# Kernel tuning notes

Measured on AMD Instinct MI355X. Metric: run time of the kernel, lower is better.

The kernel has to match this reference:

```python
import jax, jax.numpy as jnp
import numpy as np

B, F, H, W = 1, 4, 20, 44
P = H * W            # 880 tokens per frame (20*44, from max_attention_size = 15*880)
S = F * P            # 3520 packed tokens
DIM, NH, FFN, OUT = 1536, 12, 6144, 64   # OUT = prod(patch_size)*out_dim = 4*16
HD = DIM // NH       # 128
C = HD // 2          # 64 rotary complex pairs
EPS = 1e-6


def _rope_angles():
    # Wan 3D RoPE: split C pairs as (C-2*(C//3), C//3, C//3) over (frame, h, w)
    cf, ch, cw = C - 2 * (C // 3), C // 3, C // 3
    def tab(n, cp):
        inv = 1.0 / (10000.0 ** (np.arange(cp) / cp))
        return np.outer(np.arange(n), inv)
    af = np.broadcast_to(tab(F, cf)[:, None, None, :], (F, H, W, cf))
    ah = np.broadcast_to(tab(H, ch)[None, :, None, :], (F, H, W, ch))
    aw = np.broadcast_to(tab(W, cw)[None, None, :, :], (F, H, W, cw))
    return np.concatenate([af, ah, aw], -1).reshape(S, C).astype(np.float32)


def setup_inputs() -> dict:
    key = jax.random.key(0)
    ks = jax.random.split(key, 24)
    g = lambda i, shape, s=0.02: jax.random.normal(ks[i], shape, dtype=jnp.float32) * s
    inp = {
        'x': jax.random.normal(ks[0], (B, S, DIM), dtype=jnp.float32),
        'e': g(1, (B, F, 6, DIM), 1.0),
        'e_head': g(2, (B, F, 2, DIM), 1.0),
        'rope_angles': jnp.asarray(_rope_angles()),
        'mod_block': g(3, (1, 6, DIM), 1.0 / float(np.sqrt(DIM))),
        'mod_head': g(4, (1, 2, DIM), 1.0 / float(np.sqrt(DIM))),
        'Wq': g(5, (DIM, DIM)), 'bq': jnp.zeros((DIM,), jnp.float32),
        'Wk': g(6, (DIM, DIM)), 'bk': jnp.zeros((DIM,), jnp.float32),
        'Wv': g(7, (DIM, DIM)), 'bv': jnp.zeros((DIM,), jnp.float32),
        'Wo': g(8, (DIM, DIM)), 'bo': jnp.zeros((DIM,), jnp.float32),
        'wq_norm': jnp.ones((DIM,), jnp.float32),
        'wk_norm': jnp.ones((DIM,), jnp.float32),
        'W1': g(9, (DIM, FFN)), 'b1': jnp.zeros((FFN,), jnp.float32),
        'W2': g(10, (FFN, DIM)), 'b2': jnp.zeros((DIM,), jnp.float32),
        'Wh': g(11, (DIM, OUT)), 'bh': jnp.zeros((OUT,), jnp.float32),
    }
    return inp


def _ln(x):
    # WanLayerNorm without elementwise affine
    m = jnp.mean(x, axis=-1, keepdims=True)
    v = jnp.var(x, axis=-1, keepdims=True)
    return (x - m) * jax.lax.rsqrt(v + EPS)


def _rms(x, w):
    return x * jax.lax.rsqrt(jnp.mean(x * x, axis=-1, keepdims=True) + EPS) * w


def _rope(t, ang):
    # t: [B,S,NH,HD]; adjacent pairs form complex numbers (view_as_complex style)
    tr = t.reshape(B, S, NH, C, 2)
    cos = jnp.cos(ang)[None, :, None, :]
    sin = jnp.sin(ang)[None, :, None, :]
    t0, t1 = tr[..., 0], tr[..., 1]
    return jnp.stack([t0 * cos - t1 * sin, t0 * sin + t1 * cos], -1).reshape(B, S, NH, HD)


def reference(x, e, e_head, rope_angles, mod_block, mod_head,
              Wq, bq, Wk, bk, Wv, bv, Wo, bo, wq_norm, wk_norm,
              W1, b1, W2, b2, Wh, bh):
    # ---- AdaLN modulation split (6-way) ----
    em = mod_block[:, None] + e                      # [B,F,6,DIM]
    e0, e1, e2, e3, e4, e5 = [em[:, :, i][:, :, None, :] for i in range(6)]

    xf = x.reshape(B, F, P, DIM)
    h = (_ln(xf) * (1 + e1) + e0).reshape(B, S, DIM)

    # ---- QK-RMSNorm + RoPE self attention (block-causal, block = one frame) ----
    q = _rope(_rms(h @ Wq + bq, wq_norm).reshape(B, S, NH, HD), rope_angles)
    k = _rope(_rms(h @ Wk + bk, wk_norm).reshape(B, S, NH, HD), rope_angles)
    v = (h @ Wv + bv).reshape(B, S, NH, HD)

    blk = jnp.arange(S) // P
    mask = blk[None, :] <= blk[:, None]              # [S,S] block-causal
    scores = jnp.einsum('bqhd,bkhd->bhqk', q, k) / np.float32(np.sqrt(HD))
    scores = jnp.where(mask[None, None], scores, jnp.float32(-1e30))
    attn = jax.nn.softmax(scores, axis=-1)
    y = jnp.einsum('bhqk,bkhd->bqhd', attn, v).reshape(B, S, DIM) @ Wo + bo

    xf = xf + y.reshape(B, F, P, DIM) * e2

    # ---- FFN with AdaLN modulation ----
    hf = (_ln(xf) * (1 + e4) + e3).reshape(B, S, DIM)
    ff = jax.nn.gelu(hf @ W1 + b1) @ W2 + b2
    xf = xf + ff.reshape(B, F, P, DIM) * e5

    # ---- OutputHead: modulated norm + linear ----
    eh = mod_head[:, None] + e_head                  # [B,F,2,DIM]
    eh0 = eh[:, :, 0][:, :, None, :]
    eh1 = eh[:, :, 1][:, :, None, :]
    out = (_ln(xf) * (1 + eh1) + eh0) @ Wh + bh      # [B,F,P,OUT]
    return out
```

## Files before the change

### kernel.cpp

```cpp
#include <hip/hip_runtime.h>
#include <cstdint>
#include <cstddef>

typedef __bf16 bf16;
typedef __bf16 bf16x2 __attribute__((ext_vector_type(2)));
typedef __bf16 bf16x8 __attribute__((ext_vector_type(8)));
typedef float f32x4 __attribute__((ext_vector_type(4)));
typedef unsigned int u32x4 __attribute__((ext_vector_type(4)));

#define S_TOK 3520
#define S_PAD 3584
#define P_TOK 880
#define NFRM 4
#define DIM 1536
#define NH 12
#define HD 128
#define FFN_D 6144
#define NOUT 64
#define EPSV 1e-6f
#define QSCALE 0.12751743f

__device__ __forceinline__ f32x4 mfma16(bf16x8 a, bf16x8 b, f32x4 c) {
  return __builtin_amdgcn_mfma_f32_16x16x32_bf16(a, b, c, 0, 0, 0);
}

__device__ __forceinline__ void gload_lds16(const bf16* g, bf16* l) {
  __builtin_amdgcn_global_load_lds(
      (const __attribute__((address_space(1))) unsigned int*)g,
      (__attribute__((address_space(3))) unsigned int*)l, 16, 0, 0);
}

__device__ __forceinline__ uint32_t pk2(float lo, float hi) {
  bf16x2 t;
  t[0] = (bf16)lo;
  t[1] = (bf16)hi;
  return __builtin_bit_cast(uint32_t, t);
}

__global__ __launch_bounds__(256) void k_prep(const float* __restrict__ e,
                                              const float* __restrict__ e_head,
                                              const float* __restrict__ mod_block,
                                              const float* __restrict__ mod_head,
                                              float* __restrict__ em,
                                              float* __restrict__ ehm) {
  int i = blockIdx.x * 256 + threadIdx.x;
  if (i < NFRM * 6 * DIM) em[i] = mod_block[i % (6 * DIM)] + e[i];
  int j = i - NFRM * 6 * DIM;
  if (j >= 0 && j < NFRM * 2 * DIM) ehm[j] = mod_head[j % (2 * DIM)] + e_head[j];
}

__global__ __launch_bounds__(256) void k_zero_vpad(bf16* __restrict__ vc) {
  size_t base = ((size_t)blockIdx.x * 28 + 27) * 4096 + 2048 + (size_t)threadIdx.x * 8;
#pragma unroll
  for (int i = 0; i < 8; ++i) vc[base + i] = (bf16)0.f;
}

__global__ __launch_bounds__(256) void k_transpose(const float* __restrict__ W,
                                                   bf16* __restrict__ Wt, int K, int N) {
  __shared__ float tile[32][33];
  int n0 = blockIdx.x * 32, k0 = blockIdx.y * 32;
  int tx = threadIdx.x & 31, ty = threadIdx.x >> 5;
#pragma unroll
  for (int j = 0; j < 4; ++j) {
    int k = k0 + ty * 4 + j;
    float v = (n0 + tx < N) ? W[(size_t)k * N + n0 + tx] : 0.f;
    tile[ty * 4 + j][tx] = v;
  }
  __syncthreads();
#pragma unroll
  for (int j = 0; j < 4; ++j) {
    int n = n0 + ty * 4 + j;
    if (n < N) Wt[(size_t)n * K + k0 + tx] = (bf16)tile[tx][ty * 4 + j];
  }
}

__global__ __launch_bounds__(256) void k_adaln(const float* __restrict__ in,
                                               bf16* __restrict__ out,
                                               const float* __restrict__ e_shift,
                                               const float* __restrict__ e_scale,
                                               int fstride) {
  int tok = blockIdx.x;
  int t = threadIdx.x;
  bf16* orow = out + (size_t)tok * DIM;
  if (tok >= S_TOK) {
#pragma unroll
    for (int i = 0; i < 6; ++i) orow[t * 6 + i] = (bf16)0.f;
    return;
  }
  const float* xrow = in + (size_t)tok * DIM;
  float v[6];
  float s = 0.f, sq = 0.f;
#pragma unroll
  for (int i = 0; i < 6; ++i) {
    v[i] = xrow[t * 6 + i];
    s += v[i];
    sq += v[i] * v[i];
  }
  for (int off = 32; off; off >>= 1) {
    s += __shfl_down(s, off);
    sq += __shfl_down(sq, off);
  }
  __shared__ float red[8];
  int wv = t >> 6, lane = t & 63;
  if (lane == 0) { red[wv] = s; red[4 + wv] = sq; }
  __syncthreads();
  float ts = red[0] + red[1] + red[2] + red[3];
  float tq = red[4] + red[5] + red[6] + red[7];
  float mean = ts * (1.f / DIM);
  float var = tq * (1.f / DIM) - mean * mean;
  float rstd = rsqrtf(var + EPSV);
  int f = tok / P_TOK;
  const float* sh = e_shift + (size_t)f * fstride;
  const float* sc = e_scale + (size_t)f * fstride;
#pragma unroll
  for (int i = 0; i < 6; ++i) {
    int d = t * 6 + i;
    orow[d] = (bf16)((v[i] - mean) * rstd * (1.f + sc[d]) + sh[d]);
  }
}

__global__ __launch_bounds__(256) void k_qkv_post(const float* __restrict__ qkv,
                                                  const float* __restrict__ wqn,
                                                  const float* __restrict__ wkn,
                                                  const float* __restrict__ ang,
                                                  bf16* __restrict__ qb,
                                                  bf16* __restrict__ kb,
                                                  bf16* __restrict__ vc) {
  int s = blockIdx.x;
  int t = threadIdx.x;
  const float* row = qkv + (size_t)s * 3 * DIM;
  float qv[6], kv[6], vv[6];
  float sqq = 0.f, sqk = 0.f;
  int d0 = t * 6;
#pragma unroll
  for (int i = 0; i < 6; ++i) {
    int d = d0 + i;
    qv[i] = row[d];
    kv[i] = row[DIM + d];
    vv[i] = row[2 * DIM + d];
    sqq += qv[i] * qv[i];
    sqk += kv[i] * kv[i];
  }
  float a1 = sqq, a2 = sqk;
  for (int off = 32; off; off >>= 1) {
    a1 += __shfl_down(a1, off);
    a2 += __shfl_down(a2, off);
  }
  __shared__ float red[8];
  int wv = t >> 6, lane = t & 63;
  if (lane == 0) { red[wv] = a1; red[4 + wv] = a2; }
  __syncthreads();
  float tq = red[0] + red[1] + red[2] + red[3];
  float tk = red[4] + red[5] + red[6] + red[7];
  float rq = rsqrtf(tq * (1.f / DIM) + EPSV);
  float rk = rsqrtf(tk * (1.f / DIM) + EPSV);
#pragma unroll
  for (int p = 0; p < 3; ++p) {
    int d = d0 + p * 2;
    int h = d >> 7;
    int hd = d & 127;
    int c = hd >> 1;
    float a = ang[(size_t)s * 64 + c];
    float sa, ca;
    sincosf(a, &sa, &ca);
    float q0 = qv[p * 2] * rq * wqn[d], q1 = qv[p * 2 + 1] * rq * wqn[d + 1];
    float k0 = kv[p * 2] * rk * wkn[d], k1 = kv[p * 2 + 1] * rk * wkn[d + 1];
    size_t base = ((size_t)h * S_TOK + s) * HD + hd;
    qb[base]     = (bf16)((q0 * ca - q1 * sa) * QSCALE);
    qb[base + 1] = (bf16)((q0 * sa + q1 * ca) * QSCALE);
    kb[base]     = (bf16)(k0 * ca - k1 * sa);
    kb[base + 1] = (bf16)(k0 * sa + k1 * ca);
  }
  int f = s / P_TOK;
  int l = s - f * P_TOK;
  int lb = l >> 5, gg = (l >> 3) & 3, r = l & 7;
#pragma unroll
  for (int i = 0; i < 6; ++i) {
    int d = d0 + i;
    int h = d >> 7, hd = d & 127;
    vc[((((size_t)(h * NFRM + f)) * 28 + lb) * 512 + gg * 128 + hd) * 8 + r] = (bf16)vv[i];
  }
}

__global__ __launch_bounds__(320) void k_attn(const bf16* __restrict__ qb,
                                              const bf16* __restrict__ kb,
                                              const bf16* __restrict__ vc,
                                              float* __restrict__ parto,
                                              float* __restrict__ partml) {
  __shared__ __align__(16) bf16 Ks[2][512 * 8];
  __shared__ __align__(16) bf16 Vs[2][512 * 8];
  int h = blockIdx.x / 110;
  int p = blockIdx.x % 110;
  int f = (p < 11) ? 0 : (p < 33) ? 1 : (p < 66) ? 2 : 3;
  int cum = (f == 0) ? 0 : (f == 1) ? 11 : (f == 2) ? 33 : 66;
  int w = p - cum;
  int kc = w / 11;
  int qt = f * 11 + w % 11;
  int slot = blockIdx.x;
  int t = threadIdx.x;
  int wv = t >> 6, lane = t & 63;
  int r16 = lane & 15, g = lane >> 4;
  int q0 = qt * 80 + wv * 16;
  int kv0 = kc * P_TOK;
  const bf16* qbase = qb + ((size_t)h * S_TOK + q0 + r16) * HD + g * 8;
  bf16x8 qf[4];
#pragma unroll
  for (int kk = 0; kk < 4; ++kk) qf[kk] = *(const bf16x8*)(qbase + kk * 32);
  f32x4 acc[8] = {};
  float mrow = -1e30f, lrow = 0.f;
  int src01 = r16 + ((2 * g) & 3) * 16;
  int src23 = src01 + 16;
  bool glo = (g < 2);
  int sB = t + 256;
  int kr0 = t >> 4, kl0 = t & 15;
  int ks0 = (kl0 & 8) | ((kl0 ^ kr0) & 7);
  int kr1 = sB >> 4, kl1 = sB & 15;
  int ks1 = (kl1 & 8) | ((kl1 ^ kr1) & 7);
  const bf16* kh = kb + (size_t)h * S_TOK * HD;
  const bf16* vchunk = vc + ((size_t)(h * NFRM + kc)) * 28 * 4096;
#define STAGE_ATT(buf, jj)                                                  \
  do {                                                                      \
    int kvoj = (jj) * 32;                                                   \
    int gr0 = kv0 + kvoj + kr0; if (gr0 >= S_TOK) gr0 = 0;                  \
    int gr1 = kv0 + kvoj + kr1; if (gr1 >= S_TOK) gr1 = 0;                  \
    gload_lds16(kh + (size_t)gr0 * HD + ks0 * 8, Ks[buf] + t * 8);          \
    gload_lds16(kh + (size_t)gr1 * HD + ks1 * 8, Ks[buf] + sB * 8);         \
    gload_lds16(vchunk + (size_t)(jj) * 4096 + t * 8, Vs[buf] + t * 8);     \
    gload_lds16(vchunk + (size_t)(jj) * 4096 + sB * 8, Vs[buf] + sB * 8);   \
  } while (0)
  const int nsteps = (P_TOK + 31) >> 5;
  if (t < 256) STAGE_ATT(0, 0);
  int cur = 0;
  for (int j = 0; j < nsteps; ++j) {
    int kvo = j * 32;
    if (j + 1 < nsteps) {
      if (t < 256) STAGE_ATT(cur ^ 1, j + 1);
      asm volatile("s_waitcnt vmcnt(4)" ::: "memory");
    } else {
      asm volatile("s_waitcnt vmcnt(0)" ::: "memory");
    }
    __builtin_amdgcn_s_barrier();
    f32x4 st0 = {0.f, 0.f, 0.f, 0.f}, st1 = {0.f, 0.f, 0.f, 0.f};
#pragma unroll
    for (int kk = 0; kk < 4; ++kk) {
      int sl = g + 4 * kk;
      int ss = (sl & 8) | ((sl ^ r16) & 7);
      bf16x8 k0 = *(const bf16x8*)(Ks[cur] + (r16 * 16 + ss) * 8);
      bf16x8 k1 = *(const bf16x8*)(Ks[cur] + ((16 + r16) * 16 + ss) * 8);
      st0 = mfma16(k0, qf[kk], st0);
      st1 = mfma16(k1, qf[kk], st1);
    }
    float hm = (kvo + 16 >= P_TOK) ? -1e30f : 0.f;
    float a0[4], a1[4];
#pragma unroll
    for (int r = 0; r < 4; ++r) {
      a0[r] = st0[r];
      a1[r] = st1[r] + hm;
    }
    float tm = fmaxf(fmaxf(fmaxf(a0[0], a0[1]), fmaxf(a0[2], a0[3])),
                     fmaxf(fmaxf(a1[0], a1[1]), fmaxf(a1[2], a1[3])));
    tm = fmaxf(tm, __shfl_xor(tm, 16));
    tm = fmaxf(tm, __shfl_xor(tm, 32));
    float mn = fmaxf(mrow, tm);
    float p0[4], p1[4], ps = 0.f;
#pragma unroll
    for (int r = 0; r < 4; ++r) {
      p0[r] = exp2f(a0[r] - mn);
      p1[r] = exp2f(a1[r] - mn);
      ps += p0[r] + p1[r];
    }
    float scl = exp2f(mrow - mn);
    mrow = mn;
    lrow = lrow * scl + ps;
    uint32_t A0 = pk2(p0[0], p0[1]), A1 = pk2(p0[2], p0[3]);
    uint32_t B0 = pk2(p1[0], p1[1]), B1 = pk2(p1[2], p1[3]);
    uint32_t sA0 = __shfl(A0, src01), sA1 = __shfl(A1, src01);
    uint32_t sB0 = __shfl(B0, src01), sB1 = __shfl(B1, src01);
    uint32_t tA0 = __shfl(A0, src23), tA1 = __shfl(A1, src23);
    uint32_t tB0 = __shfl(B0, src23), tB1 = __shfl(B1, src23);
    u32x4 wds;
    wds[0] = glo ? sA0 : sB0;
    wds[1] = glo ? sA1 : sB1;
    wds[2] = glo ? tA0 : tB0;
    wds[3] = glo ? tA1 : tB1;
    bf16x8 pb = __builtin_bit_cast(bf16x8, wds);
#pragma unroll
    for (int hb = 0; hb < 8; ++hb) {
      acc[hb][0] *= scl;
      acc[hb][1] *= scl;
      acc[hb][2] *= scl;
      acc[hb][3] *= scl;
    }
    const bf16* vsl = Vs[cur] + (size_t)(g * 128 + r16) * 8;
#pragma unroll
    for (int hb = 0; hb < 8; ++hb) {
      bf16x8 vfr = *(const bf16x8*)(vsl + hb * 128);
      acc[hb] = mfma16(vfr, pb, acc[hb]);
    }
    asm volatile("" ::: "memory");
    __builtin_amdgcn_s_barrier();
    cur ^= 1;
  }
#undef STAGE_ATT
  lrow += __shfl_xor(lrow, 16);
  lrow += __shfl_xor(lrow, 32);
  float* obase = parto + (((size_t)slot * 5 + wv) * 8) * 256;
#pragma unroll
  for (int hb = 0; hb < 8; ++hb) {
    *(f32x4*)(obase + (hb * 64 + lane) * 4) = acc[hb];
  }
  if (g == 0) {
    float* mlb = partml + ((size_t)slot * 5 + wv) * 32;
    mlb[r16] = mrow;
    mlb[16 + r16] = lrow;
  }
}

__global__ __launch_bounds__(256) void k_att_reduce(const float* __restrict__ parto,
                                                    const float* __restrict__ partml,
                                                    bf16* __restrict__ attb) {
  int b = blockIdx.x;
  int h = b / 44, qt = b % 44;
  int f = qt / 11, j = qt % 11;
  int cum = (f == 0) ? 0 : (f == 1) ? 11 : (f == 2) ? 33 : 66;
  int t = threadIdx.x;
  int d = t & 127, half = t >> 7;
  int hb = d >> 4, g = (d >> 2) & 3, r = d & 3;
  int q0 = qt * 80;
  for (int it = 0; it < 40; ++it) {
    int qloc = it + 40 * half;
    int wv = qloc >> 4, r16 = qloc & 15;
    float m[4], l[4];
    float mt = -1e30f;
    for (int kc = 0; kc <= f; ++kc) {
      int slot = h * 110 + cum + kc * 11 + j;
      const float* mlb = partml + ((size_t)slot * 5 + wv) * 32;
      m[kc] = mlb[r16];
      l[kc] = mlb[16 + r16];
      mt = fmaxf(mt, m[kc]);
    }
    float lt = 0.f, o = 0.f;
    for (int kc = 0; kc <= f; ++kc) {
      int slot = h * 110 + cum + kc * 11 + j;
      float wgt = exp2f(m[kc] - mt);
      lt += l[kc] * wgt;
      o += parto[(((size_t)slot * 5 + wv) * 8 + hb) * 256 + (g * 16 + r16) * 4 + r] * wgt;
    }
    attb[(size_t)(q0 + qloc) * DIM + h * HD + d] = (bf16)(o / lt);
  }
}

struct Gemm256P {
  const bf16* A;
  const bf16* Bt;
  int K;
  int Mtiles;
  int Ntiles;
  int Mreal;
  int mode;
  const float* bias0;
  const float* bias1;
  const float* bias2;
  float* outf;
  bf16* outb;
  int ldo;
};

__global__ __launch_bounds__(512, 2) void k_gemm256(Gemm256P p) {
  int nwg = p.Mtiles * p.Ntiles;
  int bid = blockIdx.x;
  int xq = nwg >> 3, xr = nwg & 7;
  int xcd = bid & 7, jj = bid >> 3;
  int wg = (xcd < xr ? xcd * (xq + 1) : xr * (xq + 1) + (xcd - xr) * xq) + jj;
  int bm = wg % p.Mtiles;
  int bn = wg / p.Mtiles;
  __shared__ __align__(16) bf16 Asl[2][256 * 64];
  __shared__ __align__(16) bf16 Bsl[2][256 * 64];
  int t = threadIdx.x, lane = t & 63, wv = t >> 6;
  int r16 = lane & 15, g = lane >> 4;
  int wr = wv >> 2, wc = wv & 3;
  f32x4 acc[8][4] = {};
  const bf16* Ag = p.A + (size_t)bm * 256 * p.K;
  const bf16* Bg = p.Bt + (size_t)bn * 256 * p.K;
  int r7 = r16 & 7;
#define STAGE256(buf, kt)                                                        \
  do {                                                                           \
    int k0s = (kt) * 64;                                                         \
    _Pragma("unroll") for (int o = 0; o < 4; ++o) {                              \
      int b = o * 512 + t;                                                       \
      int rw = b >> 3;                                                           \
      int cb = (b & 7) ^ (rw & 7);                                               \
      gload_lds16(Ag + (size_t)rw * p.K + k0s + cb * 8, Asl[buf] + b * 8);       \
    }                                                                            \
    _Pragma("unroll") for (int o = 0; o < 4; ++o) {                              \
      int b = o * 512 + t;                                                       \
      int rw = b >> 3;                                                           \
      int cb = (b & 7) ^ (rw & 7);                                               \
      gload_lds16(Bg + (size_t)rw * p.K + k0s + cb * 8, Bsl[buf] + b * 8);       \
    }                                                                            \
  } while (0)
  const int nt = p.K >> 6;
  STAGE256(0, 0);
  int cur = 0;
  for (int tt = 0; tt < nt; ++tt) {
    if (tt + 1 < nt) {
      STAGE256(cur ^ 1, tt + 1);
      asm volatile("s_waitcnt vmcnt(8)" ::: "memory");
    } else {
      asm volatile("s_waitcnt vmcnt(0)" ::: "memory");
    }
    __builtin_amdgcn_s_barrier();
    const bf16* Ac = Asl[cur];
    const bf16* Bc = Bsl[cur];
#pragma unroll
    for (int q = 0; q < 4; ++q) {
      int mb0 = (q >> 1) * 4, nb0 = (q & 1) * 2;
      bf16x8 af[4][2], bfr[2][2];
#pragma unroll
      for (int mi = 0; mi < 4; ++mi)
#pragma unroll
        for (int kk = 0; kk < 2; ++kk)
          af[mi][kk] = *(const bf16x8*)(Ac + (size_t)(wr * 128 + (mb0 + mi) * 16 + r16) * 64 +
                                        (((kk * 4 + g) ^ r7) * 8));
#pragma unroll
      for (int ni = 0; ni < 2; ++ni)
#pragma unroll
        for (int kk = 0; kk < 2; ++kk)
          bfr[ni][kk] = *(const bf16x8*)(Bc + (size_t)(wc * 64 + (nb0 + ni) * 16 + r16) * 64 +
                                         (((kk * 4 + g) ^ r7) * 8));
      __builtin_amdgcn_s_setprio(1);
#pragma unroll
      for (int mi = 0; mi < 4; ++mi)
#pragma unroll
        for (int ni = 0; ni < 2; ++ni)
#pragma unroll
          for (int kk = 0; kk < 2; ++kk)
            acc[mb0 + mi][nb0 + ni] = mfma16(af[mi][kk], bfr[ni][kk], acc[mb0 + mi][nb0 + ni]);
      __builtin_amdgcn_s_setprio(0);
    }
    asm volatile("" ::: "memory");
    __builtin_amdgcn_s_barrier();
    cur ^= 1;
  }
#undef STAGE256
  int mbase = bm * 256 + wr * 128, nbase = bn * 256 + wc * 64;
#pragma unroll
  for (int mi = 0; mi < 8; ++mi) {
#pragma unroll
    for (int ni = 0; ni < 4; ++ni) {
      int col = nbase + ni * 16 + r16;
#pragma unroll
      for (int r = 0; r < 4; ++r) {
        int row = mbase + mi * 16 + 4 * g + r;
        if (row >= p.Mreal) continue;
        float v = acc[mi][ni][r];
        if (p.mode == 0) {
          float b = col < DIM ? p.bias0[col]
                              : (col < 2 * DIM ? p.bias1[col - DIM] : p.bias2[col - 2 * DIM]);
          p.outf[(size_t)row * p.ldo + col] = v + b;
        } else {
          float xg = v + p.bias0[col];
          float gl = 0.5f * xg * (1.f + tanhf(0.7978845608028654f * (xg + 0.044715f * xg * xg * xg)));
          p.outb[(size_t)row * p.ldo + col] = (bf16)gl;
        }
      }
    }
  }
}

struct GemmP {
  const bf16* A;
  const bf16* Bt;
  int K;
  int Mtiles;
  int Ntiles;
  int Mreal;
  int mode;
  const float* bias0;
  const float* bias1;
  const float* bias2;
  const float* res;
  const float* emod;
  int e_fstride;
  float* outf;
  bf16* outb;
  int ldo;
};

__global__ __launch_bounds__(256, 3) void k_gemm(GemmP p) {
  int nwg = p.Mtiles * p.Ntiles;
  int bid = blockIdx.x;
  int l = bid;
  if ((nwg & 7) == 0) {
    int cpx = nwg >> 3;
    l = (bid & 7) * cpx + (bid >> 3);
  }
  int bm = l % p.Mtiles;
  int bn = l / p.Mtiles;
  __shared__ __align__(16) bf16 As[3][128 * 32];
  __shared__ __align__(16) bf16 Bs[3][128 * 32];
  int t = threadIdx.x, lane = t & 63, wv = t >> 6;
  int r16 = lane & 15, g = lane >> 4;
  int wr = wv >> 1, wc = wv & 1;
  f32x4 acc[4][4] = {};
  const bf16* Ag = p.A + (size_t)bm * 128 * p.K;
  const bf16* Bg = p.Bt + (size_t)bn * 128 * p.K;
  int c0 = t, c1 = t + 256;
  int row0 = c0 >> 2, off0 = (c0 & 3) * 8;
  int row1 = c1 >> 2, off1 = (c1 & 3) * 8;
#define STAGE(buf, kk)                                                     \
  do {                                                                     \
    gload_lds16(Ag + (size_t)row0 * p.K + (kk) + off0, As[buf] + c0 * 8);  \
    gload_lds16(Ag + (size_t)row1 * p.K + (kk) + off1, As[buf] + c1 * 8);  \
    gload_lds16(Bg + (size_t)row0 * p.K + (kk) + off0, Bs[buf] + c0 * 8);  \
    gload_lds16(Bg + (size_t)row1 * p.K + (kk) + off1, Bs[buf] + c1 * 8);  \
  } while (0)
  const int nt = p.K >> 5;
  STAGE(0, 0);
  STAGE(1, 32);
  int cur = 0;
  for (int tt = 0; tt < nt; ++tt) {
    int rem = nt - 1 - tt;
    if (rem >= 2) {
      int nb = cur + 2;
      if (nb >= 3) nb -= 3;
      STAGE(nb, (tt + 2) * 32);
      asm volatile("s_waitcnt vmcnt(8)" ::: "memory");
    } else if (rem == 1) {
      asm volatile("s_waitcnt vmcnt(4)" ::: "memory");
    } else {
      asm volatile("s_waitcnt vmcnt(0)" ::: "memory");
    }
    __builtin_amdgcn_s_barrier();
    bf16x8 af[4], bfr[4];
#pragma unroll
    for (int mi = 0; mi < 4; ++mi)
      af[mi] = *(const bf16x8*)(As[cur] + (wr * 64 + mi * 16 + r16) * 32 + g * 8);
#pragma unroll
    for (int ni = 0; ni < 4; ++ni)
      bfr[ni] = *(const bf16x8*)(Bs[cur] + (wc * 64 + ni * 16 + r16) * 32 + g * 8);
#pragma unroll
    for (int mi = 0; mi < 4; ++mi)
#pragma unroll
      for (int ni = 0; ni < 4; ++ni)
        acc[mi][ni] = mfma16(af[mi], bfr[ni], acc[mi][ni]);
    asm volatile("" ::: "memory");
    __builtin_amdgcn_s_barrier();
    cur = (cur + 1 == 3) ? 0 : cur + 1;
  }
#undef STAGE
  int mb = bm * 128 + wr * 64, nb0 = bn * 128 + wc * 64;
#pragma unroll
  for (int mi = 0; mi < 4; ++mi) {
#pragma unroll
    for (int ni = 0; ni < 4; ++ni) {
      int col = nb0 + ni * 16 + r16;
#pragma unroll
      for (int r = 0; r < 4; ++r) {
        int row = mb + mi * 16 + 4 * g + r;
        if (row >= p.Mreal) continue;
        float v = acc[mi][ni][r];
        if (p.mode == 0) {
          float b = col < DIM ? p.bias0[col]
                              : (col < 2 * DIM ? p.bias1[col - DIM] : p.bias2[col - 2 * DIM]);
          p.outf[(size_t)row * p.ldo + col] = v + b;
        } else if (p.mode == 1) {
          int fr = row / P_TOK;
          p.outf[(size_t)row * p.ldo + col] =
              p.res[(size_t)row * DIM + col] +
              (v + p.bias0[col]) * p.emod[(size_t)fr * p.e_fstride + col];
        } else if (p.mode == 2) {
          float xg = v + p.bias0[col];
          float gl = 0.5f * xg * (1.f + tanhf(0.7978845608028654f * (xg + 0.044715f * xg * xg * xg)));
          p.outb[(size_t)row * p.ldo + col] = (bf16)gl;
        } else {
          if (col < NOUT) p.outf[(size_t)row * p.ldo + col] = v + p.bias0[col];
        }
      }
    }
  }
}

extern "C" void kernel_launch(void* const* d_in, const int* in_sizes, int n_in,
                              void* d_out, int out_size, void* d_ws, size_t ws_size,
                              hipStream_t stream) {
  const float* x = (const float*)d_in[0];
  const float* e = (const float*)d_in[1];
  const float* e_head = (const float*)d_in[2];
  const float* ang = (const float*)d_in[3];
  const float* mod_block = (const float*)d_in[4];
  const float* mod_head = (const float*)d_in[5];
  const float* Wq = (const float*)d_in[6];
  const float* bq = (const float*)d_in[7];
  const float* Wk = (const float*)d_in[8];
  const float* bk = (const float*)d_in[9];
  const float* Wv = (const float*)d_in[10];
  const float* bv = (const float*)d_in[11];
  const float* Wo = (const float*)d_in[12];
  const float* bo = (const float*)d_in[13];
  const float* wqn = (const float*)d_in[14];
  const float* wkn = (const float*)d_in[15];
  const float* W1 = (const float*)d_in[16];
  const float* b1 = (const float*)d_in[17];
  const float* W2 = (const float*)d_in[18];
  const float* b2 = (const float*)d_in[19];
  const float* Wh = (const float*)d_in[20];
  const float* bh = (const float*)d_in[21];
  float* out = (float*)d_out;
  char* ws = (char*)d_ws;

  size_t WT_QKV = 0;
  size_t WT_O = WT_QKV + (size_t)3 * DIM * DIM * 2;
  size_t W1T = WT_O + (size_t)DIM * DIM * 2;
  size_t W2T = W1T + (size_t)FFN_D * DIM * 2;
  size_t WHT = W2T + (size_t)DIM * FFN_D * 2;
  size_t EMOFF = WHT + (size_t)128 * DIM * 2;
  size_t EHOFF = EMOFF + (size_t)NFRM * 6 * DIM * 4;
  size_t HB = EHOFF + (size_t)NFRM * 2 * DIM * 4;
  size_t CQKV = HB + (size_t)S_PAD * DIM * 2;
  size_t DQB = CQKV + (size_t)S_TOK * 3 * DIM * 4;
  size_t EATT = DQB + (size_t)3 * NH * S_TOK * HD * 2;
  size_t GXF2 = EATT + (size_t)S_PAD * DIM * 2;
  size_t END = GXF2 + (size_t)S_TOK * DIM * 4;
  if (ws_size < END) return;

  bf16* wtqkv = (bf16*)(ws + WT_QKV);
  bf16* wto = (bf16*)(ws + WT_O);
  bf16* w1t = (bf16*)(ws + W1T);
  bf16* w2t = (bf16*)(ws + W2T);
  bf16* wht = (bf16*)(ws + WHT);
  float* em = (float*)(ws + EMOFF);
  float* ehm = (float*)(ws + EHOFF);
  bf16* hb = (bf16*)(ws + HB);
  float* qkvf = (float*)(ws + CQKV);
  bf16* ffb = (bf16*)(ws + CQKV);
  float* parto = (float*)(ws + CQKV);
  float* partml = parto + (size_t)1320 * 5 * 8 * 256;
  bf16* qbp = (bf16*)(ws + DQB);
  bf16* kbp = qbp + (size_t)NH * S_TOK * HD;
  bf16* vcp = kbp + (size_t)NH * S_TOK * HD;
  float* xf3 = (float*)(ws + DQB);
  bf16* attb = (bf16*)(ws + EATT);
  float* xf2 = (float*)(ws + GXF2);

  k_prep<<<(NFRM * 8 * DIM) / 256, 256, 0, stream>>>(e, e_head, mod_block, mod_head, em, ehm);
  k_zero_vpad<<<NH * NFRM, 256, 0, stream>>>(vcp);

  k_transpose<<<dim3(48, 48), 256, 0, stream>>>(Wq, wtqkv, DIM, DIM);
  k_transpose<<<dim3(48, 48), 256, 0, stream>>>(Wk, wtqkv + (size_t)DIM * DIM, DIM, DIM);
  k_transpose<<<dim3(48, 48), 256, 0, stream>>>(Wv, wtqkv + (size_t)2 * DIM * DIM, DIM, DIM);
  k_transpose<<<dim3(48, 48), 256, 0, stream>>>(Wo, wto, DIM, DIM);
  k_transpose<<<dim3(192, 48), 256, 0, stream>>>(W1, w1t, DIM, FFN_D);
  k_transpose<<<dim3(48, 192), 256, 0, stream>>>(W2, w2t, FFN_D, DIM);
  k_transpose<<<dim3(2, 48), 256, 0, stream>>>(Wh, wht, DIM, NOUT);
  hipMemsetAsync(ws + WHT + (size_t)NOUT * DIM * 2, 0, (size_t)(128 - NOUT) * DIM * 2, stream);
  hipMemsetAsync(ws + EATT + (size_t)S_TOK * DIM * 2, 0, (size_t)(S_PAD - S_TOK) * DIM * 2, stream);

  k_adaln<<<S_PAD, 256, 0, stream>>>(x, hb, em, em + DIM, 6 * DIM);

  Gemm256P q0{};
  q0.A = hb; q0.Bt = wtqkv; q0.K = DIM; q0.Mtiles = 14; q0.Ntiles = 18; q0.Mreal = S_TOK;
  q0.mode = 0; q0.bias0 = bq; q0.bias1 = bk; q0.bias2 = bv; q0.outf = qkvf; q0.ldo = 3 * DIM;
  k_gemm256<<<14 * 18, 512, 0, stream>>>(q0);

  k_qkv_post<<<S_TOK, 256, 0, stream>>>(qkvf, wqn, wkn, ang, qbp, kbp, vcp);

  k_attn<<<NH * 110, 320, 0, stream>>>(qbp, kbp, vcp, parto, partml);
  k_att_reduce<<<NH * 44, 256, 0, stream>>>(parto, partml, attb);

  GemmP g1{};
  g1.A = attb; g1.Bt = wto; g1.K = DIM; g1.Mtiles = 28; g1.Ntiles = 12; g1.Mreal = S_TOK;
  g1.mode = 1; g1.bias0 = bo; g1.res = x; g1.emod = em + 2 * DIM; g1.e_fstride = 6 * DIM;
  g1.outf = xf2; g1.ldo = DIM;
  k_gemm<<<28 * 12, 256, 0, stream>>>(g1);

  k_adaln<<<S_PAD, 256, 0, stream>>>(xf2, hb, em + 3 * DIM, em + 4 * DIM, 6 * DIM);

  Gemm256P q2{};
  q2.A = hb; q2.Bt = w1t; q2.K = DIM; q2.Mtiles = 14; q2.Ntiles = 24; q2.Mreal = S_TOK;
  q2.mode = 2; q2.bias0 = b1; q2.outb = ffb; q2.ldo = FFN_D;
  k_gemm256<<<14 * 24, 512, 0, stream>>>(q2);
  hipMemsetAsync(ws + CQKV + (size_t)S_TOK * FFN_D * 2, 0, (size_t)(S_PAD - S_TOK) * FFN_D * 2, stream);

  GemmP g3{};
  g3.A = ffb; g3.Bt = w2t; g3.K = FFN_D; g3.Mtiles = 28; g3.Ntiles = 12; g3.Mreal = S_TOK;
  g3.mode = 1; g3.bias0 = b2; g3.res = xf2; g3.emod = em + 5 * DIM; g3.e_fstride = 6 * DIM;
  g3.outf = xf3; g3.ldo = DIM;
  k_gemm<<<28 * 12, 256, 0, stream>>>(g3);

  k_adaln<<<S_PAD, 256, 0, stream>>>(xf3, hb, ehm, ehm + DIM, 2 * DIM);

  GemmP g4{};
  g4.A = hb; g4.Bt = wht; g4.K = DIM; g4.Mtiles = 28; g4.Ntiles = 1; g4.Mreal = S_TOK;
  g4.mode = 4; g4.bias0 = bh; g4.outf = out; g4.ldo = NOUT;
  k_gemm<<<28, 256, 0, stream>>>(g4);
}
```

Before: 817.1 us.

## Interleave next-tile global-to-LDS loads with MFMA quadrants in 256 GEMM

```diff
diff --git a/kernel.cpp b/kernel.cpp
--- a/kernel.cpp
+++ b/kernel.cpp
@@ -378,71 +378,89 @@
   __shared__ __align__(16) bf16 Bsl[2][256 * 64];
   int t = threadIdx.x, lane = t & 63, wv = t >> 6;
   int r16 = lane & 15, g = lane >> 4;
+  int s7 = r16 & 7;
   int wr = wv >> 2, wc = wv & 3;
   f32x4 acc[8][4] = {};
   const bf16* Ag = p.A + (size_t)bm * 256 * p.K;
   const bf16* Bg = p.Bt + (size_t)bn * 256 * p.K;
-  int r7 = r16 & 7;
-#define STAGE256(buf, kt)                                                        \
+#define STAGEH(d, kt, h)                                                         \
   do {                                                                           \
     int k0s = (kt) * 64;                                                         \
-    _Pragma("unroll") for (int o = 0; o < 4; ++o) {                              \
+    const bf16* src = ((h) < 2 ? Ag : Bg);                                       \
+    bf16* dst = ((h) < 2 ? Asl[d] : Bsl[d]) + ((h) & 1) * (128 * 64);            \
+    int rbase = ((h) & 1) * 128;                                                 \
+    _Pragma("unroll") for (int o = 0; o < 2; ++o) {                              \
       int b = o * 512 + t;                                                       \
       int rw = b >> 3;                                                           \
       int cb = (b & 7) ^ (rw & 7);                                               \
-      gload_lds16(Ag + (size_t)rw * p.K + k0s + cb * 8, Asl[buf] + b * 8);       \
-    }                                                                            \
-    _Pragma("unroll") for (int o = 0; o < 4; ++o) {                              \
-      int b = o * 512 + t;                                                       \
-      int rw = b >> 3;                                                           \
-      int cb = (b & 7) ^ (rw & 7);                                               \
-      gload_lds16(Bg + (size_t)rw * p.K + k0s + cb * 8, Bsl[buf] + b * 8);       \
+      gload_lds16(src + (size_t)(rbase + rw) * p.K + k0s + cb * 8, dst + b * 8); \
     }                                                                            \
   } while (0)
+  bf16x8 af[4][2], bfr[4][2];
+#define RD_A(Ac, MB)                                                             \
+  _Pragma("unroll") for (int mi = 0; mi < 4; ++mi)                               \
+  _Pragma("unroll") for (int kk = 0; kk < 2; ++kk)                               \
+    af[mi][kk] = *(const bf16x8*)((Ac) + (size_t)(wr * 128 + (MB) + mi * 16 + r16) * 64 + \
+                                  (((kk * 4 + g) ^ s7) * 8));
+#define RD_B(Bc, NB)                                                             \
+  _Pragma("unroll") for (int ni = 0; ni < 2; ++ni)                               \
+  _Pragma("unroll") for (int kk = 0; kk < 2; ++kk)                               \
+    bfr[(NB) + ni][kk] = *(const bf16x8*)((Bc) + (size_t)(wc * 64 + ((NB) + ni) * 16 + r16) * 64 + \
+                                          (((kk * 4 + g) ^ s7) * 8));
+#define QUAD(MB, NB)                                                             \
+  __builtin_amdgcn_s_setprio(1);                                                 \
+  _Pragma("unroll") for (int mi = 0; mi < 4; ++mi)                               \
+  _Pragma("unroll") for (int ni = 0; ni < 2; ++ni)                               \
+  _Pragma("unroll") for (int kk = 0; kk < 2; ++kk)                               \
+    acc[(MB) / 16 + mi][(NB) + ni] = mfma16(af[mi][kk], bfr[(NB) + ni][kk],      \
+                                            acc[(MB) / 16 + mi][(NB) + ni]);     \
+  __builtin_amdgcn_s_setprio(0);
   const int nt = p.K >> 6;
-  STAGE256(0, 0);
+  STAGEH(0, 0, 0);
+  STAGEH(0, 0, 1);
+  STAGEH(0, 0, 2);
+  STAGEH(0, 0, 3);
   int cur = 0;
   for (int tt = 0; tt < nt; ++tt) {
-    if (tt + 1 < nt) {
-      STAGE256(cur ^ 1, tt + 1);
-      asm volatile("s_waitcnt vmcnt(8)" ::: "memory");
+    const bf16* Ac = Asl[cur];
+    const bf16* Bc = Bsl[cur];
+    int nb = cur ^ 1;
+    bool more = (tt + 1 < nt);
+    if (more) {
+      STAGEH(nb, tt + 1, 0);
+      asm volatile("s_waitcnt vmcnt(2)" ::: "memory");
     } else {
       asm volatile("s_waitcnt vmcnt(0)" ::: "memory");
     }
     __builtin_amdgcn_s_barrier();
-    const bf16* Ac = Asl[cur];
-    const bf16* Bc = Bsl[cur];
-#pragma unroll
-    for (int q = 0; q < 4; ++q) {
-      int mb0 = (q >> 1) * 4, nb0 = (q & 1) * 2;
-      bf16x8 af[4][2], bfr[2][2];
-#pragma unroll
-      for (int mi = 0; mi < 4; ++mi)
-#pragma unroll
-        for (int kk = 0; kk < 2; ++kk)
-          af[mi][kk] = *(const bf16x8*)(Ac + (size_t)(wr * 128 + (mb0 + mi) * 16 + r16) * 64 +
-                                        (((kk * 4 + g) ^ r7) * 8));
-#pragma unroll
-      for (int ni = 0; ni < 2; ++ni)
-#pragma unroll
-        for (int kk = 0; kk < 2; ++kk)
-          bfr[ni][kk] = *(const bf16x8*)(Bc + (size_t)(wc * 64 + (nb0 + ni) * 16 + r16) * 64 +
-                                         (((kk * 4 + g) ^ r7) * 8));
-      __builtin_amdgcn_s_setprio(1);
-#pragma unroll
-      for (int mi = 0; mi < 4; ++mi)
-#pragma unroll
-        for (int ni = 0; ni < 2; ++ni)
-#pragma unroll
-          for (int kk = 0; kk < 2; ++kk)
-            acc[mb0 + mi][nb0 + ni] = mfma16(af[mi][kk], bfr[ni][kk], acc[mb0 + mi][nb0 + ni]);
-      __builtin_amdgcn_s_setprio(0);
-    }
+    RD_A(Ac, 0);
+    RD_B(Bc, 0);
+    QUAD(0, 0);
     asm volatile("" ::: "memory");
     __builtin_amdgcn_s_barrier();
+    RD_B(Bc, 2);
+    if (more) STAGEH(nb, tt + 1, 1);
+    __builtin_amdgcn_s_barrier();
+    QUAD(0, 2);
+    asm volatile("" ::: "memory");
+    __builtin_amdgcn_s_barrier();
+    RD_A(Ac, 64);
+    if (more) STAGEH(nb, tt + 1, 2);
+    __builtin_amdgcn_s_barrier();
+    QUAD(64, 0);
+    asm volatile("" ::: "memory");
+    __builtin_amdgcn_s_barrier();
+    if (more) STAGEH(nb, tt + 1, 3);
+    __builtin_amdgcn_s_barrier();
+    QUAD(64, 2);
+    asm volatile("" ::: "memory");
+    __builtin_amdgcn_s_barrier();
     cur ^= 1;
   }
-#undef STAGE256
+#undef QUAD
+#undef RD_B
+#undef RD_A
+#undef STAGEH
   int mbase = bm * 256 + wr * 128, nbase = bn * 256 + wc * 64;
 #pragma unroll
   for (int mi = 0; mi < 8; ++mi) {
```

Result: no change. 808.2 us (-1.1%).
